# Kernel tuning notes

Hardware: AMD Instinct MI355X
Metric: run time of the kernel (lower is better)

The kernel has to match this reference:

```python
import jax, jax.numpy as jnp
import numpy as np

IGNORE_INDEX = -100
VOCAB = 32000
D_MODEL = 2048


def setup_inputs() -> dict:
    key = jax.random.key(0)
    k1, k2, k3 = jax.random.split(key, 3)
    outputs = jax.random.normal(k1, (4, 2048, D_MODEL), dtype=jnp.float32)
    targets = jax.random.randint(k2, (4, 2048), 0, VOCAB, dtype=jnp.int64)
    # LM-head projection weight (torch nn.Linear stores [out_features, in_features]; no bias for LM heads)
    weight = jax.random.normal(k3, (VOCAB, D_MODEL), dtype=jnp.float32) * (D_MODEL ** -0.5)
    return {"outputs": outputs, "targets": targets, "weight": weight}


def reference(outputs, targets, weight):
    # Flatten tokens: [B, S, D] -> [N, D], [B, S] -> [N]
    d = outputs.shape[-1]
    hidden = outputs.reshape(-1, d)
    tgt = targets.reshape(-1)
    valid = tgt != IGNORE_INDEX
    safe_tgt = jnp.where(valid, tgt, 0)

    # Linear projection fused conceptually with CE; per-chunk sum-reduction CE
    # summed over chunks equals the full-batch sum, so we compute it vectorized.
    logits = jnp.einsum("nd,vd->nv", hidden, weight).astype(jnp.float32)  # [N, V]
    logp = jax.nn.log_softmax(logits, axis=-1)
    nll = -jnp.take_along_axis(logp, safe_tgt[:, None], axis=-1)[:, 0]  # [N]

    total_valid = jnp.sum(valid)
    total_loss = jnp.sum(jnp.where(valid, nll, 0.0))
    # forward returns 0.0 when no valid tokens; guard the division
    return jnp.where(total_valid > 0, total_loss / jnp.maximum(total_valid, 1).astype(total_loss.dtype), 0.0)
```

## Files before the change

### kernel.cpp

```cpp
#include <hip/hip_runtime.h>
#include <hip/hip_bf16.h>
#include <math.h>

#define D_MODEL 2048
#define VOCAB   32000
#define NTOK    8192
#define BM      128
#define BN      128
#define BKB     128
#define BK      32
#define LDK     (BK + 8)
#define MTILES  (NTOK / BM)
#define NTILES  (VOCAB / BN)
#define NCHUNK  (VOCAB / 64)

typedef __attribute__((ext_vector_type(8))) short  frag8;
typedef __attribute__((ext_vector_type(4))) float  f32x4;
typedef __attribute__((ext_vector_type(4))) int    i32x4;
typedef __attribute__((ext_vector_type(8))) int    i32x8;


__device__ inline void g2l16(const void* g, void* l) {
    __builtin_amdgcn_global_load_lds(
        (const __attribute__((address_space(1))) unsigned int*)g,
        (__attribute__((address_space(3))) unsigned int*)l,
        16, 0, 0);
}

__device__ inline unsigned pack_bf16(float x, float y) {
    union { float f; unsigned u; } a, b;
    a.f = x; b.f = y;
    return __builtin_amdgcn_perm(b.u, a.u, 0x07060302u);
}


__global__ void cvt_fp8_kernel(const float* __restrict__ src, unsigned char* __restrict__ dst) {
    size_t i = (size_t)blockIdx.x * 256 + threadIdx.x;
    float4 v0 = ((const float4*)src)[2 * i];
    float4 v1 = ((const float4*)src)[2 * i + 1];
    int lo = 0, hi = 0;
    lo = __builtin_amdgcn_cvt_pk_fp8_f32(v0.x, v0.y, lo, 0);
    lo = __builtin_amdgcn_cvt_pk_fp8_f32(v0.z, v0.w, lo, 1);
    hi = __builtin_amdgcn_cvt_pk_fp8_f32(v1.x, v1.y, hi, 0);
    hi = __builtin_amdgcn_cvt_pk_fp8_f32(v1.z, v1.w, hi, 1);
    uint2 o = { (unsigned)lo, (unsigned)hi };
    ((uint2*)dst)[i] = o;
}


__global__ __launch_bounds__(256, 3)
void gemm_lse_fp8(const unsigned char* __restrict__ Hq, const unsigned char* __restrict__ Wq,
                  float* __restrict__ partials) {
    __shared__ unsigned char As[BM * BKB];
    __shared__ unsigned char Bs[BN * BKB];

    const int bid   = blockIdx.x;
    const int mtile = bid & (MTILES - 1);
    const int ntile = bid >> 6;
    const int m0 = mtile * BM;
    const int n0 = ntile * BN;

    const int tid  = threadIdx.x;
    const int lane = tid & 63;
    const int w    = tid >> 6;
    const int wm   = (w >> 1) * 64;
    const int wn   = (w & 1)  * 64;
    const int q    = lane >> 4;
    const int c    = lane & 15;

    const int srow = w * 32 + (lane >> 3);
    const int soff = ((lane & 7) ^ (srow & 7)) * 16;
    const unsigned char* gA = Hq + (size_t)(m0 + srow) * D_MODEL + soff;
    const unsigned char* gB = Wq + (size_t)(n0 + srow) * D_MODEL + soff;
    unsigned char* lA = As + (w * 32) * BKB;
    unsigned char* lB = Bs + (w * 32) * BKB;

    const int plo = (2 * q) ^ (c & 7);

    f32x4 acc[4][4];
    const f32x4 zero = {0.f, 0.f, 0.f, 0.f};
    #pragma unroll
    for (int i = 0; i < 4; ++i)
        #pragma unroll
        for (int j = 0; j < 4; ++j) acc[i][j] = zero;

    #pragma unroll 1
    for (int kt = 0; kt < D_MODEL / BKB; ++kt) {
        const size_t k0 = (size_t)kt * BKB;
        #pragma unroll
        for (int t = 0; t < 4; ++t)
            g2l16(gA + k0 + (size_t)(t * 8) * D_MODEL, lA + t * 8 * BKB);
        #pragma unroll
        for (int t = 0; t < 4; ++t)
            g2l16(gB + k0 + (size_t)(t * 8) * D_MODEL, lB + t * 8 * BKB);
        __syncthreads();

        union Frag { i32x8 v; i32x4 h[2]; };
        i32x8 a8[4], b8[4];
        #pragma unroll
        for (int t = 0; t < 4; ++t) {
            const unsigned char* pa = As + (wm + t * 16 + c) * BKB;
            Frag f;
            f.h[0] = *(const i32x4*)(pa + plo * 16);
            f.h[1] = *(const i32x4*)(pa + (plo ^ 1) * 16);
            a8[t] = f.v;
        }
        #pragma unroll
        for (int t = 0; t < 4; ++t) {
            const unsigned char* pb = Bs + (wn + t * 16 + c) * BKB;
            Frag f;
            f.h[0] = *(const i32x4*)(pb + plo * 16);
            f.h[1] = *(const i32x4*)(pb + (plo ^ 1) * 16);
            b8[t] = f.v;
        }

        #pragma unroll
        for (int tm = 0; tm < 4; ++tm)
            #pragma unroll
            for (int tn = 0; tn < 4; ++tn)
                acc[tm][tn] = __builtin_amdgcn_mfma_scale_f32_16x16x128_f8f6f4(
                    a8[tm], b8[tn], acc[tm][tn],
                    0, 0,
                    0, 0x7F7F7F7F,
                    0, 0x7F7F7F7F);
        __syncthreads();
    }

    const int chunk = ntile * 2 + (w & 1);
    #pragma unroll
    for (int tm = 0; tm < 4; ++tm) {
        #pragma unroll
        for (int r = 0; r < 4; ++r) {
            float v0 = acc[tm][0][r], v1 = acc[tm][1][r];
            float v2 = acc[tm][2][r], v3 = acc[tm][3][r];
            float mx = fmaxf(fmaxf(v0, v1), fmaxf(v2, v3));
            #pragma unroll
            for (int mask = 1; mask <= 8; mask <<= 1)
                mx = fmaxf(mx, __shfl_xor(mx, mask, 64));
            float sm = __expf(v0 - mx) + __expf(v1 - mx)
                     + __expf(v2 - mx) + __expf(v3 - mx);
            #pragma unroll
            for (int mask = 1; mask <= 8; mask <<= 1)
                sm += __shfl_xor(sm, mask, 64);
            if (c == 0) {
                int row_g = m0 + wm + tm * 16 + q * 4 + r;
                float* p = partials + ((size_t)row_g * NCHUNK + chunk) * 2;
                p[0] = mx;
                p[1] = sm;
            }
        }
    }
}


__global__ __launch_bounds__(256, 2)
void gemm_lse_f32(const float* __restrict__ H, const float* __restrict__ W,
                  float* __restrict__ partials) {
    __shared__ unsigned short As[BM][LDK];
    __shared__ unsigned short Bs[BN][LDK];

    const int GM = 8;
    int bid   = blockIdx.x;
    int super = bid / (GM * NTILES);
    int rem   = bid % (GM * NTILES);
    int mtile = super * GM + (rem % GM);
    int ntile = rem / GM;

    const int m0 = mtile * BM;
    const int n0 = ntile * BN;

    const int tid  = threadIdx.x;
    const int lane = tid & 63;
    const int w    = tid >> 6;
    const int wm   = (w >> 1) * 64;
    const int wn   = (w & 1)  * 64;
    const int q    = lane >> 4;
    const int c    = lane & 15;

    f32x4 acc[4][4];
    const f32x4 zero = {0.f, 0.f, 0.f, 0.f};
    #pragma unroll
    for (int i = 0; i < 4; ++i)
        #pragma unroll
        for (int j = 0; j < 4; ++j) acc[i][j] = zero;

    for (int kt = 0; kt < D_MODEL / BK; ++kt) {
        const int k0 = kt * BK;
        #pragma unroll
        for (int s = 0; s < 4; ++s) {
            int i   = tid + s * 256;
            int row = i >> 3;
            int kq  = (i & 7) << 2;

            const float4* pa = (const float4*)(H + (size_t)(m0 + row) * D_MODEL + k0 + kq);
            float4 va = *pa;
            uint2 ba = { pack_bf16(va.x, va.y), pack_bf16(va.z, va.w) };
            *(uint2*)&As[row][kq] = ba;

            const float4* pb = (const float4*)(W + (size_t)(n0 + row) * D_MODEL + k0 + kq);
            float4 vb = *pb;
            uint2 bb = { pack_bf16(vb.x, vb.y), pack_bf16(vb.z, vb.w) };
            *(uint2*)&Bs[row][kq] = bb;
        }
        __syncthreads();

        frag8 af[4], bf[4];
        #pragma unroll
        for (int t = 0; t < 4; ++t)
            af[t] = *(const frag8*)&As[wm + t * 16 + c][q * 8];
        #pragma unroll
        for (int t = 0; t < 4; ++t)
            bf[t] = *(const frag8*)&Bs[wn + t * 16 + c][q * 8];

        #pragma unroll
        for (int tm = 0; tm < 4; ++tm)
            #pragma unroll
            for (int tn = 0; tn < 4; ++tn)
                acc[tm][tn] = __builtin_amdgcn_mfma_f32_16x16x32_bf16(
                    af[tm], bf[tn], acc[tm][tn], 0, 0, 0);
        __syncthreads();
    }

    const int chunk = ntile * 2 + (w & 1);
    #pragma unroll
    for (int tm = 0; tm < 4; ++tm) {
        #pragma unroll
        for (int r = 0; r < 4; ++r) {
            float v0 = acc[tm][0][r], v1 = acc[tm][1][r];
            float v2 = acc[tm][2][r], v3 = acc[tm][3][r];
            float mx = fmaxf(fmaxf(v0, v1), fmaxf(v2, v3));
            #pragma unroll
            for (int mask = 1; mask <= 8; mask <<= 1)
                mx = fmaxf(mx, __shfl_xor(mx, mask, 64));
            float sm = __expf(v0 - mx) + __expf(v1 - mx)
                     + __expf(v2 - mx) + __expf(v3 - mx);
            #pragma unroll
            for (int mask = 1; mask <= 8; mask <<= 1)
                sm += __shfl_xor(sm, mask, 64);
            if (c == 0) {
                int row_g = m0 + wm + tm * 16 + q * 4 + r;
                float* p = partials + ((size_t)row_g * NCHUNK + chunk) * 2;
                p[0] = mx;
                p[1] = sm;
            }
        }
    }
}


__global__ void tgt_kernel(const float* __restrict__ H, const float* __restrict__ W,
                           const int* __restrict__ targets,
                           float* __restrict__ tgt_logit, float* __restrict__ accum) {
    int token = blockIdx.x;
    int tid   = threadIdx.x;
    if (token == 0 && tid == 0) { accum[0] = 0.f; accum[1] = 0.f; }

    int t  = targets[token];
    int tt = (t == -100) ? 0 : t;
    const float4* h  = (const float4*)(H + (size_t)token * D_MODEL);
    const float4* wr = (const float4*)(W + (size_t)tt * D_MODEL);
    float p = 0.f;
    for (int j = tid; j < D_MODEL / 4; j += 256) {
        float4 a = h[j], b = wr[j];
        p += a.x * b.x + a.y * b.y + a.z * b.z + a.w * b.w;
    }
    #pragma unroll
    for (int mask = 1; mask < 64; mask <<= 1)
        p += __shfl_xor(p, mask, 64);

    __shared__ float lp[4];
    int lane = tid & 63, wid = tid >> 6;
    if (lane == 0) lp[wid] = p;
    __syncthreads();
    if (tid == 0) tgt_logit[token] = lp[0] + lp[1] + lp[2] + lp[3];
}

__device__ inline void lse_merge(float& m, float& s, float om, float os) {
    if (om > m) { s = s * __expf(m - om) + os; m = om; }
    else        { s += os * __expf(om - m); }
}

__global__ void reduce_kernel(const float* __restrict__ partials,
                              const float* __restrict__ tgt_logit,
                              const int* __restrict__ targets,
                              float* __restrict__ accum) {
    int token = blockIdx.x;
    int tid   = threadIdx.x;
    float m = -INFINITY, s = 0.f;
    for (int ch = tid; ch < NCHUNK; ch += 256) {
        const float* p = partials + ((size_t)token * NCHUNK + ch) * 2;
        lse_merge(m, s, p[0], p[1]);
    }
    #pragma unroll
    for (int mask = 1; mask < 64; mask <<= 1) {
        float om = __shfl_xor(m, mask, 64);
        float os = __shfl_xor(s, mask, 64);
        lse_merge(m, s, om, os);
    }
    __shared__ float lm[4], ls[4];
    int lane = tid & 63, wid = tid >> 6;
    if (lane == 0) { lm[wid] = m; ls[wid] = s; }
    __syncthreads();
    if (tid == 0) {
        for (int i = 1; i < 4; ++i) lse_merge(m, s, lm[i], ls[i]);
        float lse = m + __logf(s);
        int t = targets[token];
        if (t != -100) {
            atomicAdd(&accum[0], lse - tgt_logit[token]);
            atomicAdd(&accum[1], 1.0f);
        }
    }
}

__global__ void final_kernel(const float* __restrict__ accum, float* __restrict__ out) {
    float L = accum[0], C = accum[1];
    out[0] = (C > 0.f) ? (L / C) : 0.f;
}


extern "C" void kernel_launch(void* const* d_in, const int* in_sizes, int n_in,
                              void* d_out, int out_size, void* d_ws, size_t ws_size,
                              hipStream_t stream) {
    (void)in_sizes; (void)n_in; (void)out_size;
    const float* H       = (const float*)d_in[0];
    const int*   targets = (const int*)d_in[1];
    const float* W       = (const float*)d_in[2];
    float*       out     = (float*)d_out;

    char* ws = (char*)d_ws;
    const size_t H8_BYTES   = (size_t)NTOK  * D_MODEL;
    const size_t W8_BYTES   = (size_t)VOCAB * D_MODEL;
    const size_t PART_BYTES = (size_t)NTOK * NCHUNK * 2 * 4;
    const size_t NEED = H8_BYTES + W8_BYTES + PART_BYTES + (size_t)NTOK * 4 + 64;

    if (ws_size >= NEED) {
        unsigned char* Hq = (unsigned char*)ws;
        unsigned char* Wq = (unsigned char*)(ws + H8_BYTES);
        float* partials   = (float*)(ws + H8_BYTES + W8_BYTES);
        float* tgt_logit  = (float*)(ws + H8_BYTES + W8_BYTES + PART_BYTES);
        float* accum      = tgt_logit + NTOK;

        cvt_fp8_kernel<<<(NTOK  * D_MODEL / 8) / 256, 256, 0, stream>>>(H, Hq);
        cvt_fp8_kernel<<<(VOCAB * D_MODEL / 8) / 256, 256, 0, stream>>>(W, Wq);
        tgt_kernel<<<NTOK, 256, 0, stream>>>(H, W, targets, tgt_logit, accum);
        gemm_lse_fp8<<<MTILES * NTILES, 256, 0, stream>>>(Hq, Wq, partials);
        reduce_kernel<<<NTOK, 256, 0, stream>>>(partials, tgt_logit, targets, accum);
        final_kernel<<<1, 1, 0, stream>>>(accum, out);
    } else {
        float* partials  = (float*)ws;
        float* tgt_logit = (float*)(ws + PART_BYTES);
        float* accum     = tgt_logit + NTOK;

        gemm_lse_f32<<<MTILES * NTILES, 256, 0, stream>>>(H, W, partials);
        tgt_kernel<<<NTOK, 256, 0, stream>>>(H, W, targets, tgt_logit, accum);
        reduce_kernel<<<NTOK, 256, 0, stream>>>(partials, tgt_logit, targets, accum);
        final_kernel<<<1, 1, 0, stream>>>(accum, out);
    }
}
```

Measured before the change: 1.181 ms.

## Use one wavefront per token in target and reduce kernels, drop atomics

The target-logit and LSE-reduce kernels now assign one 64-lane wavefront per token, four tokens per block, instead of a whole 256-thread block per token. This removes the shared-memory cross-wave step and the __syncthreads. Per-token NLL values are written to a buffer and summed by a 256-thread final kernel, replacing the global float atomics. The target kernel is also moved after the GEMM. These kernels are small next to the GEMM, so any gain is limited, and the workspace requirement grows slightly.

```diff
diff --git a/kernel.cpp b/kernel.cpp
--- a/kernel.cpp
+++ b/kernel.cpp
@@ -248,31 +248,26 @@
 }
 
 
-__global__ void tgt_kernel(const float* __restrict__ H, const float* __restrict__ W,
-                           const int* __restrict__ targets,
-                           float* __restrict__ tgt_logit, float* __restrict__ accum) {
-    int token = blockIdx.x;
-    int tid   = threadIdx.x;
-    if (token == 0 && tid == 0) { accum[0] = 0.f; accum[1] = 0.f; }
+__global__ __launch_bounds__(256)
+void tgt_kernel(const float* __restrict__ H, const float* __restrict__ W,
+                const int* __restrict__ targets, float* __restrict__ tgt_logit) {
+    int token = blockIdx.x * 4 + (threadIdx.x >> 6);
+    int lane  = threadIdx.x & 63;
 
     int t  = targets[token];
     int tt = (t == -100) ? 0 : t;
     const float4* h  = (const float4*)(H + (size_t)token * D_MODEL);
     const float4* wr = (const float4*)(W + (size_t)tt * D_MODEL);
     float p = 0.f;
-    for (int j = tid; j < D_MODEL / 4; j += 256) {
+    #pragma unroll
+    for (int j = lane; j < D_MODEL / 4; j += 64) {
         float4 a = h[j], b = wr[j];
         p += a.x * b.x + a.y * b.y + a.z * b.z + a.w * b.w;
     }
     #pragma unroll
     for (int mask = 1; mask < 64; mask <<= 1)
         p += __shfl_xor(p, mask, 64);
-
-    __shared__ float lp[4];
-    int lane = tid & 63, wid = tid >> 6;
-    if (lane == 0) lp[wid] = p;
-    __syncthreads();
-    if (tid == 0) tgt_logit[token] = lp[0] + lp[1] + lp[2] + lp[3];
+    if (lane == 0) tgt_logit[token] = p;
 }
 
 __device__ inline void lse_merge(float& m, float& s, float om, float os) {
@@ -280,16 +275,19 @@
     else        { s += os * __expf(om - m); }
 }
 
-__global__ void reduce_kernel(const float* __restrict__ partials,
-                              const float* __restrict__ tgt_logit,
-                              const int* __restrict__ targets,
-                              float* __restrict__ accum) {
-    int token = blockIdx.x;
-    int tid   = threadIdx.x;
+__global__ __launch_bounds__(256)
+void reduce_kernel(const float* __restrict__ partials,
+                   const float* __restrict__ tgt_logit,
+                   const int* __restrict__ targets,
+                   float* __restrict__ nll) {
+    int token = blockIdx.x * 4 + (threadIdx.x >> 6);
+    int lane  = threadIdx.x & 63;
+
     float m = -INFINITY, s = 0.f;
-    for (int ch = tid; ch < NCHUNK; ch += 256) {
-        const float* p = partials + ((size_t)token * NCHUNK + ch) * 2;
-        lse_merge(m, s, p[0], p[1]);
+    const float* base = partials + (size_t)token * NCHUNK * 2;
+    for (int ch = lane; ch < NCHUNK; ch += 64) {
+        float2 p = ((const float2*)base)[ch];
+        lse_merge(m, s, p.x, p.y);
     }
     #pragma unroll
     for (int mask = 1; mask < 64; mask <<= 1) {
@@ -297,24 +295,35 @@
         float os = __shfl_xor(s, mask, 64);
         lse_merge(m, s, om, os);
     }
-    __shared__ float lm[4], ls[4];
+    if (lane == 0) {
+        int t = targets[token];
+        nll[token] = (t != -100) ? (m + __logf(s) - tgt_logit[token]) : 0.0f;
+    }
+}
+
+__global__ __launch_bounds__(256)
+void final_kernel(const float* __restrict__ nll, const int* __restrict__ targets,
+                  float* __restrict__ out) {
+    int tid = threadIdx.x;
+    float sum = 0.f, cnt = 0.f;
+    for (int i = tid; i < NTOK; i += 256) {
+        sum += nll[i];
+        cnt += (targets[i] != -100) ? 1.0f : 0.0f;
+    }
+    #pragma unroll
+    for (int mask = 1; mask < 64; mask <<= 1) {
+        sum += __shfl_xor(sum, mask, 64);
+        cnt += __shfl_xor(cnt, mask, 64);
+    }
+    __shared__ float lsum[4], lcnt[4];
     int lane = tid & 63, wid = tid >> 6;
-    if (lane == 0) { lm[wid] = m; ls[wid] = s; }
+    if (lane == 0) { lsum[wid] = sum; lcnt[wid] = cnt; }
     __syncthreads();
     if (tid == 0) {
-        for (int i = 1; i < 4; ++i) lse_merge(m, s, lm[i], ls[i]);
-        float lse = m + __logf(s);
-        int t = targets[token];
-        if (t != -100) {
-            atomicAdd(&accum[0], lse - tgt_logit[token]);
-            atomicAdd(&accum[1], 1.0f);
-        }
-    }
-}
-
-__global__ void final_kernel(const float* __restrict__ accum, float* __restrict__ out) {
-    float L = accum[0], C = accum[1];
-    out[0] = (C > 0.f) ? (L / C) : 0.f;
+        float S = lsum[0] + lsum[1] + lsum[2] + lsum[3];
+        float C = lcnt[0] + lcnt[1] + lcnt[2] + lcnt[3];
+        out[0] = (C > 0.f) ? (S / C) : 0.f;
+    }
 }
 
 
@@ -331,29 +340,29 @@
     const size_t H8_BYTES   = (size_t)NTOK  * D_MODEL;
     const size_t W8_BYTES   = (size_t)VOCAB * D_MODEL;
     const size_t PART_BYTES = (size_t)NTOK * NCHUNK * 2 * 4;
-    const size_t NEED = H8_BYTES + W8_BYTES + PART_BYTES + (size_t)NTOK * 4 + 64;
+    const size_t NEED = H8_BYTES + W8_BYTES + PART_BYTES + (size_t)NTOK * 8 + 64;
 
     if (ws_size >= NEED) {
         unsigned char* Hq = (unsigned char*)ws;
         unsigned char* Wq = (unsigned char*)(ws + H8_BYTES);
         float* partials   = (float*)(ws + H8_BYTES + W8_BYTES);
         float* tgt_logit  = (float*)(ws + H8_BYTES + W8_BYTES + PART_BYTES);
-        float* accum      = tgt_logit + NTOK;
+        float* nll        = tgt_logit + NTOK;
 
         cvt_fp8_kernel<<<(NTOK  * D_MODEL / 8) / 256, 256, 0, stream>>>(H, Hq);
         cvt_fp8_kernel<<<(VOCAB * D_MODEL / 8) / 256, 256, 0, stream>>>(W, Wq);
-        tgt_kernel<<<NTOK, 256, 0, stream>>>(H, W, targets, tgt_logit, accum);
         gemm_lse_fp8<<<MTILES * NTILES, 256, 0, stream>>>(Hq, Wq, partials);
-        reduce_kernel<<<NTOK, 256, 0, stream>>>(partials, tgt_logit, targets, accum);
-        final_kernel<<<1, 1, 0, stream>>>(accum, out);
+        tgt_kernel<<<NTOK / 4, 256, 0, stream>>>(H, W, targets, tgt_logit);
+        reduce_kernel<<<NTOK / 4, 256, 0, stream>>>(partials, tgt_logit, targets, nll);
+        final_kernel<<<1, 256, 0, stream>>>(nll, targets, out);
     } else {
         float* partials  = (float*)ws;
         float* tgt_logit = (float*)(ws + PART_BYTES);
-        float* accum     = tgt_logit + NTOK;
+        float* nll       = tgt_logit + NTOK;
 
         gemm_lse_f32<<<MTILES * NTILES, 256, 0, stream>>>(H, W, partials);
-        tgt_kernel<<<NTOK, 256, 0, stream>>>(H, W, targets, tgt_logit, accum);
-        reduce_kernel<<<NTOK, 256, 0, stream>>>(partials, tgt_logit, targets, accum);
-        final_kernel<<<1, 1, 0, stream>>>(accum, out);
-    }
-}
+        tgt_kernel<<<NTOK / 4, 256, 0, stream>>>(H, W, targets, tgt_logit);
+        reduce_kernel<<<NTOK / 4, 256, 0, stream>>>(partials, tgt_logit, targets, nll);
+        final_kernel<<<1, 256, 0, stream>>>(nll, targets, out);
+    }
+}
```

New measurement: 975.1 us. -17.4%, faster.
